# Performance work log

Measured on AMD Instinct MI355X. Metric: run time of the kernel, lower is better.

## Reference

```python
import jax, jax.numpy as jnp
from jax import lax
import numpy as np

MAX_D = 4  # max_displacement


def conv3x3(x, w, b):
    # x: [B,Cin,H,W], w: [Cout,Cin,3,3], SAME padding (pad=1)
    y = lax.conv_general_dilated(
        x, w, window_strides=(1, 1), padding='SAME',
        dimension_numbers=('NCHW', 'OIHW', 'NCHW'))
    return y + b[None, :, None, None]


def compute_cost_volume(f1, f2, d):
    # roll+mask in the torch code == shift with zero padding:
    # cv[idx,h,w] = mean_c f1[c,h,w] * f2[c,h-i,w-j] (zero outside bounds)
    B, C, H, W = f1.shape
    pad = jnp.pad(f2, ((0, 0), (0, 0), (d, d), (d, d)))
    slices = []
    for i in range(-d, d + 1):
        for j in range(-d, d + 1):
            shifted = lax.dynamic_slice(pad, (0, 0, d - i, d - j), (B, C, H, W))
            slices.append((f1 * shifted).sum(axis=1) / C)  # [B,H,W]
    return jnp.stack(slices, axis=1)  # [B,81,H,W]


def setup_inputs() -> dict:
    key = jax.random.key(0)
    ks = jax.random.split(key, 10)
    B, C, H, W = 16, 64, 128, 128
    cv_ch = (2 * MAX_D + 1) ** 2  # 81
    def w_init(k, shape):
        fan_in = shape[1] * shape[2] * shape[3]
        return jax.random.normal(k, shape, dtype=jnp.float32) * np.float32(np.sqrt(2.0 / fan_in))
    return {
        'f1': jax.random.normal(ks[0], (B, C, H, W), dtype=jnp.float32),
        'f2_warped': jax.random.normal(ks[1], (B, C, H, W), dtype=jnp.float32),
        'w1': w_init(ks[2], (128, C + cv_ch, 3, 3)),
        'b1': jnp.zeros((128,), dtype=jnp.float32),
        'w2': w_init(ks[3], (64, 128, 3, 3)),
        'b2': jnp.zeros((64,), dtype=jnp.float32),
        'w3': w_init(ks[4], (32, 64, 3, 3)),
        'b3': jnp.zeros((32,), dtype=jnp.float32),
        'w4': w_init(ks[5], (2, 32, 3, 3)),
        'b4': jnp.zeros((2,), dtype=jnp.float32),
    }


def reference(f1, f2_warped, w1, b1, w2, b2, w3, b3, w4, b4):
    cv = compute_cost_volume(f1, f2_warped, MAX_D)       # [B,81,H,W]
    x = jnp.concatenate([f1, cv], axis=1)                # [B,145,H,W]
    x = jax.nn.relu(conv3x3(x, w1, b1))
    x = jax.nn.relu(conv3x3(x, w2, b2))
    x = jax.nn.relu(conv3x3(x, w3, b3))
    flow = conv3x3(x, w4, b4)                            # [B,2,H,W]
    return flow
```

## Files before the change

kernel.cpp:

```cpp
#include <hip/hip_runtime.h>


typedef __bf16 bf16x8 __attribute__((ext_vector_type(8)));
typedef float f32x4 __attribute__((ext_vector_type(4)));

__device__ __forceinline__ unsigned short f2bf_bits(float f) {
  unsigned int u = __float_as_uint(f);
  unsigned int r = (u + 0x7FFFu + ((u >> 16) & 1u)) >> 16;
  return (unsigned short)r;
}

__device__ __forceinline__ void glds16(const ushort* gp, ushort* lp) {
  __builtin_amdgcn_global_load_lds((const __attribute__((address_space(1))) void*)gp,
                                   (__attribute__((address_space(3))) void*)lp, 16, 0, 0);
}

__global__ void prep_w_kernel(const float* __restrict__ w, uint4* __restrict__ wp,
                              int CIN, int COUT, int CHUNKS, int NFRAG) {
  int idx = blockIdx.x * 256 + threadIdx.x;
  int total = CHUNKS * 9 * NFRAG * 64;
  if (idx >= total) return;
  int lane = idx & 63;
  int fi = idx >> 6;
  int nf = fi % NFRAG;
  int t = fi / NFRAG;
  int rs = t % 9;
  int c = t / 9;
  int co = nf * 16 + (lane & 15);
  int cib = c * 32 + (lane >> 4) * 8;
  union { uint4 q; ushort s[8]; } pk;
#pragma unroll
  for (int e = 0; e < 8; ++e) {
    int ci = cib + e;
    float v = (ci < CIN && co < COUT) ? w[(co * CIN + ci) * 9 + rs] : 0.f;
    pk.s[e] = f2bf_bits(v);
  }
  wp[idx] = pk.q;
}

__global__ __launch_bounds__(256) void pack_f1_kernel(const float* __restrict__ f1,
                                                      ushort* __restrict__ xf1) {
  __shared__ float tile[64][132];
  const int bid = blockIdx.x;
  const int h = bid & 127, b = bid >> 7;
  const int tid = threadIdx.x;
  for (int e = tid; e < 64 * 128; e += 256) {
    int c = e >> 7, w = e & 127;
    tile[c][w] = f1[((b * 64 + c) * 128 + h) * 128 + w];
  }
  __syncthreads();
  const int px = tid >> 1, cgb = (tid & 1) * 4;
  const long base = ((long)(b * 128 + h) * 128 + px) * 64;
#pragma unroll
  for (int e = 0; e < 4; ++e) {
    int c0 = (cgb + e) * 8;
    union { uint4 q; ushort s[8]; } pk;
#pragma unroll
    for (int k = 0; k < 8; ++k) pk.s[k] = f2bf_bits(tile[c0 + k][px]);
    *reinterpret_cast<uint4*>(&xf1[base + c0]) = pk.q;
  }
}

__global__ __launch_bounds__(256)
void cost_volume_mfma_kernel(const ushort* __restrict__ xf1,
                             const ushort* __restrict__ xf2,
                             ushort* __restrict__ xcv) {
  const int bx = blockIdx.x;
  const int idx = bx >> 3;
  const int b = 2 * (bx & 7) + (idx >> 7);
  const int h = idx & 127;
  const int tid = threadIdx.x;
  const int lane = tid & 63;
  const int g = tid >> 6;
  const int l15 = lane & 15;
  const int lg = lane >> 4;

  __shared__ __align__(16) float sC[4][2][16][33];
  __shared__ __align__(16) ushort sO[96][132];

  {
    uint4 z = make_uint4(0u, 0u, 0u, 0u);
    uint4* p = (uint4*)sO;
#pragma unroll
    for (int j = 0; j < 7; ++j) {
      int e = tid + j * 256;
      if (e < 1584) p[e] = z;
    }
  }
  __syncthreads();

  const int w0g = g * 32;
  bf16x8 afr[2][2];
  {
    const ushort* f1p = xf1 + ((long)(b * 128 + h) * 128) * 64;
#pragma unroll
    for (int wt = 0; wt < 2; ++wt)
#pragma unroll
      for (int kc = 0; kc < 2; ++kc) {
        int pix = w0g + wt * 16 + l15;
        afr[wt][kc] = *reinterpret_cast<const bf16x8*>(f1p + pix * 64 + kc * 32 + lg * 8);
      }
  }

  const float inv = 1.0f / 64.0f;
  for (int A = 0; A < 9; ++A) {
    int fr = h - 4 + A;
    if ((unsigned)fr >= 128u) continue;
    const ushort* f2p = xf2 + ((long)(b * 128 + fr) * 128) * 64;
    bf16x8 bfr[3][2];
#pragma unroll
    for (int t = 0; t < 3; ++t)
#pragma unroll
      for (int kc = 0; kc < 2; ++kc) {
        int p = w0g - 4 + t * 16 + l15;
        uint4 v = make_uint4(0u, 0u, 0u, 0u);
        if ((unsigned)p < 128u)
          v = *reinterpret_cast<const uint4*>(f2p + (long)p * 64 + kc * 32 + lg * 8);
        bfr[t][kc] = __builtin_bit_cast(bf16x8, v);
      }
#pragma unroll
    for (int wt = 0; wt < 2; ++wt)
#pragma unroll
      for (int nt = 0; nt < 2; ++nt) {
        f32x4 acc = {0.f, 0.f, 0.f, 0.f};
        acc = __builtin_amdgcn_mfma_f32_16x16x32_bf16(afr[wt][0], bfr[wt + nt][0], acc, 0, 0, 0);
        acc = __builtin_amdgcn_mfma_f32_16x16x32_bf16(afr[wt][1], bfr[wt + nt][1], acc, 0, 0, 0);
#pragma unroll
        for (int j = 0; j < 4; ++j)
          sC[g][wt][lg * 4 + j][nt * 16 + l15] = acc[j];
      }
    const int chb = (8 - A) * 9;
#pragma unroll
    for (int wt = 0; wt < 2; ++wt) {
      int px = w0g + wt * 16 + l15;
#pragma unroll
      for (int u = 0; u < 3; ++u) {
        if (u < ((lg == 3) ? 3 : 2)) {
          int tj = lg * 2 + u;
          float v = sC[g][wt][l15][l15 + 8 - tj];
          sO[chb + tj][px] = f2bf_bits(v * inv);
        }
      }
    }
  }
  __syncthreads();

  uint4* dst = reinterpret_cast<uint4*>(xcv + ((long)(b * 128 + h) * 128) * 96);
#pragma unroll
  for (int j = 0; j < 6; ++j) {
    int t8 = j * 256 + tid;
    int px = t8 / 12;
    int ch0 = (t8 - px * 12) * 8;
    union { uint4 qq; ushort ss[8]; } pk;
#pragma unroll
    for (int k = 0; k < 8; ++k) pk.ss[k] = sO[ch0 + k][px];
    dst[t8] = pk.qq;
  }
}

template <int CA, int CB, int COUT, bool RELU, bool PLANAR>
__global__ __launch_bounds__(512, 2)
void conv_mfma_kernel(const ushort* __restrict__ xa, const ushort* __restrict__ xb,
                      const uint4* __restrict__ wp, const float* __restrict__ bias,
                      void* __restrict__ outv) {
  constexpr int CHUNKS = (CA + CB) / 32;
  constexpr int NFRAG = COUT / 16;
  constexpr int NFW = (NFRAG >= 2) ? NFRAG / 2 : 1;
  constexpr int MFW = (NFRAG >= 2) ? 4 : 2;
  constexpr int SXN = 4 * 130 * 32;
  constexpr int WTQ = 9 * NFRAG * 64;
  constexpr int WTA_Q = 5 * NFRAG * 64;
  constexpr int WTB_Q = 4 * NFRAG * 64;
  constexpr int WIA = (WTA_Q + 511) / 512;
  constexpr int WIB = (WTB_Q + 511) / 512;
  constexpr int SO_STRIDE = COUT + 4;
  constexpr int STAGE_B = PLANAR ? 2048 : 2 * 128 * SO_STRIDE * 2;
  constexpr int SX_B = 2 * SXN * 2;
  constexpr int BASE_B = SX_B + (WTA_Q + WTB_Q) * 16;
  constexpr int ARENA_B = STAGE_B > BASE_B ? STAGE_B : BASE_B;

  __shared__ __align__(16) char arena[ARENA_B];
  ushort* sXa = (ushort*)arena;
  ushort* sWtA = (ushort*)(arena + SX_B);
  ushort* sWtB = (ushort*)(arena + SX_B + WTA_Q * 16);

  const int bx = blockIdx.x;
  const int idx = bx >> 3;
  const int b = 2 * (bx & 7) + (idx >> 6);
  const int h0 = (idx & 63) * 2;
  const int tid = threadIdx.x;
  const int lane = tid & 63;
  const int wid = tid >> 6;
  const int l15 = lane & 15;
  const int lg = lane >> 4;
  const int cg    = (NFRAG >= 2) ? (wid >> 2) : 0;
  const int row   = (NFRAG >= 2) ? ((wid >> 1) & 1) : (wid >> 2);
  const int pbase = (NFRAG >= 2) ? ((wid & 1) * 64) : ((wid & 3) * 32);
  const bool act_wave = ((unsigned)(h0 - 1 + (wid >> 1)) < 128u);

  f32x4 acc[MFW][NFW];
#pragma unroll
  for (int mf = 0; mf < MFW; ++mf)
#pragma unroll
    for (int nf = 0; nf < NFW; ++nf) acc[mf][nf] = {0.f, 0.f, 0.f, 0.f};

  if (tid < 64) {
    int bi = tid >> 5, tr = (tid >> 3) & 3, wz = (tid >> 2) & 1, gq = tid & 3;
    int wl = wz ? 129 : 0;
    *reinterpret_cast<uint4*>(&sXa[bi * SXN + ((tr * 130 + wl) * 4 + gq) * 8]) =
        make_uint4(0u, 0u, 0u, 0u);
  }
  if (h0 == 0 || h0 == 126) {
    const int trz = (h0 == 0) ? 0 : 3;
#pragma unroll
    for (int e = 0; e < 2; ++e) {
      int u = tid + e * 512;
      int bi = u >> 9, k = u & 511;
      *reinterpret_cast<uint4*>(&sXa[bi * SXN + ((trz * 130 + 1) * 4 + k) * 8]) =
          make_uint4(0u, 0u, 0u, 0u);
    }
  }

  auto stage = [&](int c, int bi) {
    const int c0 = c * 32;
    const ushort* src;
    int cst, coff;
    if (CB == 0 || c0 < CA) { src = xa; cst = CA; coff = c0; }
    else                    { src = xb; cst = CB; coff = c0 - CA; }
    const int tr = wid >> 1;
    const int gh = h0 - 1 + tr;
    if ((unsigned)gh < 128u) {
      const ushort* rowp = src + ((long)(b * 128 + gh) * 128) * cst + coff;
#pragma unroll
      for (int t = 0; t < 4; ++t) {
        int s = (wid & 1) * 4 + t;
        int u = s * 64 + lane;
        int wl = 1 + (u >> 2);
        int gq = lane & 3;
        int sw = (wl + (wl >> 2)) & 3;
        const ushort* gp = rowp + (long)(wl - 1) * cst + (gq ^ sw) * 8;
        ushort* lp = &sXa[bi * SXN + ((tr * 130 + 1) * 4 + s * 64) * 8];
        glds16(gp, lp);
      }
    }
  };

  auto stage_wtA = [&](int c) {
    const ushort* src = (const ushort*)(wp + (size_t)c * WTQ);
#pragma unroll
    for (int i = 0; i < WIA; ++i) {
      int e = tid + i * 512;
      if ((WTA_Q % 512) == 0 || e < WTA_Q)
        glds16(src + (size_t)e * 8, sWtA + (size_t)(tid & ~63) * 8 + (size_t)(i * 512) * 8);
    }
  };
  auto stage_wtB = [&](int c) {
    const ushort* src = (const ushort*)(wp + (size_t)c * WTQ + WTA_Q);
#pragma unroll
    for (int i = 0; i < WIB; ++i) {
      int e = tid + i * 512;
      if ((WTB_Q % 512) == 0 || e < WTB_Q)
        glds16(src + (size_t)e * 8, sWtB + (size_t)(tid & ~63) * 8 + (size_t)(i * 512) * 8);
    }
  };

  auto compute = [&](int bi, int rs0, int rs1, const ushort* wbuf) {
#pragma unroll
    for (int rs = rs0; rs < rs1; ++rs) {
      const int r = rs / 3, s = rs % 3;
      const int tr = row + r;
      bf16x8 afr[MFW];
#pragma unroll
      for (int mf = 0; mf < MFW; ++mf) {
        int wl = pbase + mf * 16 + l15 + s;
        int sw = (wl + (wl >> 2)) & 3;
        afr[mf] = *reinterpret_cast<const bf16x8*>(
            &sXa[bi * SXN + ((tr * 130 + wl) * 4 + (lg ^ sw)) * 8]);
      }
      const ushort* wrow = wbuf + (size_t)((rs - rs0) * NFRAG + cg * NFW) * 64 * 8;
#pragma unroll
      for (int nf = 0; nf < NFW; ++nf) {
        bf16x8 bfr = *reinterpret_cast<const bf16x8*>(wrow + (nf * 64 + lane) * 8);
#pragma unroll
        for (int mf = 0; mf < MFW; ++mf)
          acc[mf][nf] = __builtin_amdgcn_mfma_f32_16x16x32_bf16(afr[mf], bfr, acc[mf][nf], 0, 0, 0);
      }
    }
  };

  stage(0, 0);
  stage_wtA(0);
  __syncthreads();

  for (int c = 0; c < CHUNKS; ++c) {
    const int bi = c & 1;
    stage_wtB(c);
    const bool act_issued = (c + 1 < CHUNKS) && act_wave;
    if (c + 1 < CHUNKS) stage(c + 1, bi ^ 1);
    compute(bi, 0, 5, sWtA);
    if (act_issued) asm volatile("s_waitcnt vmcnt(4)" ::: "memory");
    else            asm volatile("s_waitcnt vmcnt(0)" ::: "memory");
    __builtin_amdgcn_s_barrier();
    asm volatile("" ::: "memory");
    if (c + 1 < CHUNKS) stage_wtA(c + 1);
    compute(bi, 5, 9, sWtB);
    asm volatile("s_waitcnt vmcnt(0)" ::: "memory");
    __builtin_amdgcn_s_barrier();
    asm volatile("" ::: "memory");
  }

  if (!PLANAR) {
    ushort* sO = (ushort*)arena;
#pragma unroll
    for (int nf = 0; nf < NFW; ++nf) {
      float bs = bias[cg * NFW * 16 + nf * 16 + l15];
#pragma unroll
      for (int mf = 0; mf < MFW; ++mf) {
        int px2 = row * 128 + pbase + mf * 16 + lg * 4;
#pragma unroll
        for (int j = 0; j < 4; ++j) {
          float v = acc[mf][nf][j] + bs;
          if (RELU) v = fmaxf(v, 0.f);
          sO[(px2 + j) * SO_STRIDE + cg * NFW * 16 + nf * 16 + l15] = f2bf_bits(v);
        }
      }
    }
    __syncthreads();
    constexpr int QPP = COUT / 8;
    uint4* dst = reinterpret_cast<uint4*>((ushort*)outv + ((long)(b * 128 + h0) * 128) * COUT);
#pragma unroll
    for (int t0 = 0; t0 < 2 * 128 * QPP / 512; ++t0) {
      int t = t0 * 512 + tid;
      int px2 = t / QPP;
      int ch0 = (t & (QPP - 1)) * 8;
      union { uint4 qq; ushort ss[8]; } pk;
#pragma unroll
      for (int k = 0; k < 8; ++k) pk.ss[k] = sO[px2 * SO_STRIDE + ch0 + k];
      dst[t] = pk.qq;
    }
  } else {
    float* sF = (float*)arena;
    if (l15 < 2) {
#pragma unroll
      for (int mf = 0; mf < MFW; ++mf) {
        int pxb = pbase + mf * 16 + lg * 4;
#pragma unroll
        for (int j = 0; j < 4; ++j)
          sF[(l15 * 2 + row) * 128 + pxb + j] = acc[mf][0][j] + bias[l15];
      }
    }
    __syncthreads();
    float* out = (float*)outv;
    if (tid < 128) {
      int ch = tid >> 6, r = (tid >> 5) & 1, qx = tid & 31;
      *reinterpret_cast<float4*>(&out[((long)(b * 2 + ch) * 128 + h0 + r) * 128 + qx * 4]) =
          *reinterpret_cast<float4*>(&sF[(ch * 2 + r) * 128 + qx * 4]);
    }
  }
}

extern "C" void kernel_launch(void* const* d_in, const int* in_sizes, int n_in,
                              void* d_out, int out_size, void* d_ws, size_t ws_size,
                              hipStream_t stream) {
  (void)in_sizes; (void)n_in; (void)out_size; (void)ws_size;
  const float* f1 = (const float*)d_in[0];
  const float* f2 = (const float*)d_in[1];
  const float* w1 = (const float*)d_in[2];
  const float* b1 = (const float*)d_in[3];
  const float* w2 = (const float*)d_in[4];
  const float* b2 = (const float*)d_in[5];
  const float* w3 = (const float*)d_in[6];
  const float* b3 = (const float*)d_in[7];
  const float* w4 = (const float*)d_in[8];
  const float* b4 = (const float*)d_in[9];

  char* ws = (char*)d_ws;
  size_t off = 0;
  ushort* xf1 = (ushort*)(ws + off); off += (size_t)262144 * 64 * 2;
  ushort* xcv = (ushort*)(ws + off); off += (size_t)262144 * 96 * 2;
  ushort* x1  = (ushort*)(ws + off); off += (size_t)262144 * 128 * 2;
  ushort* x2  = (ushort*)(ws + off); off += (size_t)262144 * 64 * 2;
  uint4* wp1 = (uint4*)(ws + off); off += (size_t)5 * 9 * 8 * 64 * 16;
  uint4* wp2 = (uint4*)(ws + off); off += (size_t)4 * 9 * 4 * 64 * 16;
  uint4* wp3 = (uint4*)(ws + off); off += (size_t)2 * 9 * 2 * 64 * 16;
  uint4* wp4 = (uint4*)(ws + off); off += (size_t)1 * 9 * 1 * 64 * 16;
  ushort* x3  = xf1;
  ushort* xf2 = x1;

  prep_w_kernel<<<90, 256, 0, stream>>>(w1, wp1, 145, 128, 5, 8);
  prep_w_kernel<<<36, 256, 0, stream>>>(w2, wp2, 128, 64, 4, 4);
  prep_w_kernel<<<9, 256, 0, stream>>>(w3, wp3, 64, 32, 2, 2);
  prep_w_kernel<<<3, 256, 0, stream>>>(w4, wp4, 32, 2, 1, 1);

  pack_f1_kernel<<<2048, 256, 0, stream>>>(f1, xf1);
  pack_f1_kernel<<<2048, 256, 0, stream>>>(f2, xf2);
  cost_volume_mfma_kernel<<<2048, 256, 0, stream>>>(xf1, xf2, xcv);

  conv_mfma_kernel<64, 96, 128, true, false><<<1024, 512, 0, stream>>>(xf1, xcv, wp1, b1, x1);
  conv_mfma_kernel<128, 0, 64, true, false><<<1024, 512, 0, stream>>>(x1, x1, wp2, b2, x2);
  conv_mfma_kernel<64, 0, 32, true, false><<<1024, 512, 0, stream>>>(x2, x2, wp3, b3, x3);
  conv_mfma_kernel<32, 0, 16, false, true><<<1024, 512, 0, stream>>>(x3, x3, wp4, b4, d_out);
}
```

Baseline: 308.0 us.

## Add 4-row conv MFMA kernel with per-tap-row weight double buffering for layers 1-2

Adds a new conv kernel in which each block computes 4 output rows by 64 output channels, staging 6 input rows per 32-channel chunk. Weights are streamed one filter row (3 taps) at a time into double-buffered LDS. Layer 1 is split into two 64-channel halves, and layer 2 runs with half as many blocks. The aim is to reuse each staged activation row across more output rows and to raise MFMA work per weight and activation load, at the cost of extra barriers per chunk. The old kernel's partial vmcnt wait is also replaced with plain __syncthreads, which gives up some load/compute overlap in layers 3-4.

After: 310.6 us. No clear change (+0.8%).

```diff
diff --git a/kernel.cpp b/kernel.cpp
--- a/kernel.cpp
+++ b/kernel.cpp
@@ -155,6 +155,165 @@
 #pragma unroll
     for (int k = 0; k < 8; ++k) pk.ss[k] = sO[ch0 + k][px];
     dst[t8] = pk.qq;
+  }
+}
+
+template <int CA, int CB, int COUT_TOTAL, int HALVES, bool RELU>
+__global__ __launch_bounds__(512, 2)
+void conv_mfma4_kernel(const ushort* __restrict__ xa, const ushort* __restrict__ xb,
+                       const uint4* __restrict__ wp, const float* __restrict__ bias,
+                       ushort* __restrict__ out) {
+  constexpr int CHUNKS = (CA + CB) / 32;
+  constexpr int NFRAGT = COUT_TOTAL / 16;
+
+  __shared__ __align__(16) char arena[74496];
+  uint4* sAct = (uint4*)arena;
+  uint4* sWt = (uint4*)(arena + 49920);
+
+  const int bx = blockIdx.x;
+  const int idx = bx >> 3;
+  int wc, hq, b;
+  if (HALVES == 2) { wc = idx & 1; hq = (idx >> 1) & 31; b = 2 * (bx & 7) + (idx >> 6); }
+  else             { wc = 0;       hq = idx & 31;        b = 2 * (bx & 7) + (idx >> 5); }
+  const int h0 = hq * 4;
+  const int tid = threadIdx.x;
+  const int lane = tid & 63;
+  const int wid = tid >> 6;
+  const int row = wid >> 1;
+  const int ph = wid & 1;
+  const int l15 = lane & 15;
+  const int lg = lane >> 4;
+
+  f32x4 acc[4][4];
+#pragma unroll
+  for (int mf = 0; mf < 4; ++mf)
+#pragma unroll
+    for (int nf = 0; nf < 4; ++nf) acc[mf][nf] = {0.f, 0.f, 0.f, 0.f};
+
+  if (tid < 48) {
+    int tr = tid >> 3, wz = (tid >> 2) & 1, g = tid & 3;
+    sAct[tr * 520 + (wz ? 129 : 0) * 4 + g] = make_uint4(0u, 0u, 0u, 0u);
+  }
+  if (h0 == 0 || h0 == 124) {
+    int trz = (h0 == 0) ? 0 : 5;
+    for (int e = tid; e < 520; e += 512)
+      sAct[trz * 520 + e] = make_uint4(0u, 0u, 0u, 0u);
+  }
+
+  auto stage_act = [&](int c) {
+    const int c0 = c * 32;
+    const ushort* src; int cst, coff;
+    if (CB == 0 || c0 < CA) { src = xa; cst = CA; coff = c0; }
+    else                    { src = xb; cst = CB; coff = c0 - CA; }
+#pragma unroll
+    for (int i = 0; i < 6; ++i) {
+      int sidx = wid + i * 8;
+      int tr = sidx >> 3;
+      int seg = sidx & 7;
+      int gh = h0 - 1 + tr;
+      if ((unsigned)gh < 128u) {
+        int wl = 1 + seg * 16 + (lane >> 2);
+        int g = lane & 3;
+        int sw = (wl + (wl >> 2)) & 3;
+        const ushort* gp = src + ((long)(b * 128 + gh) * 128 + (wl - 1)) * cst + coff + (g ^ sw) * 8;
+        glds16(gp, (ushort*)(sAct + (tr * 520 + 4 + seg * 64)));
+      }
+    }
+  };
+
+  auto stage_wt = [&](int c, int p, int bufsel) {
+    const uint4* srcb = wp + ((size_t)(c * 9 + p * 3) * NFRAGT + wc * 4) * 64;
+#pragma unroll
+    for (int i = 0; i < 2; ++i) {
+      int e = tid + i * 512;
+      if (e < 768) {
+        int rsl = e >> 8;
+        int t = e & 255;
+        glds16((const ushort*)(srcb + (size_t)rsl * (NFRAGT * 64) + t),
+               (ushort*)(sWt + bufsel * 768 + (e & ~63)));
+      }
+    }
+  };
+
+  auto compute = [&](int p, int bufsel) {
+    const int tr = row + p;
+#pragma unroll
+    for (int q = 0; q < 3; ++q) {
+      bf16x8 afr[4];
+#pragma unroll
+      for (int mf = 0; mf < 4; ++mf) {
+        int wl = ph * 64 + mf * 16 + l15 + q;
+        int sw = (wl + (wl >> 2)) & 3;
+        afr[mf] = *reinterpret_cast<const bf16x8*>(
+            (const ushort*)(sAct + ((tr * 130 + wl) * 4 + (lg ^ sw))));
+      }
+      const uint4* wpiece = sWt + bufsel * 768 + q * 256;
+#pragma unroll
+      for (int nf = 0; nf < 4; ++nf) {
+        bf16x8 bfr = __builtin_bit_cast(bf16x8, wpiece[nf * 64 + lane]);
+#pragma unroll
+        for (int mf = 0; mf < 4; ++mf)
+          acc[mf][nf] = __builtin_amdgcn_mfma_f32_16x16x32_bf16(afr[mf], bfr, acc[mf][nf], 0, 0, 0);
+      }
+    }
+  };
+
+  stage_act(0);
+  stage_wt(0, 0, 0);
+  asm volatile("s_waitcnt vmcnt(0)" ::: "memory");
+  __builtin_amdgcn_s_barrier();
+  asm volatile("" ::: "memory");
+
+  for (int c = 0; c < CHUNKS; ++c) {
+    const int P0 = (3 * c) & 1, P1 = (3 * c + 1) & 1;
+    stage_wt(c, 1, P1);
+    compute(0, P0);
+    asm volatile("s_waitcnt vmcnt(0)" ::: "memory");
+    __builtin_amdgcn_s_barrier();
+    asm volatile("" ::: "memory");
+    stage_wt(c, 2, P0);
+    compute(1, P1);
+    asm volatile("s_waitcnt vmcnt(0)" ::: "memory");
+    __builtin_amdgcn_s_barrier();
+    asm volatile("" ::: "memory");
+    if (c + 1 < CHUNKS) stage_wt(c + 1, 0, P1);
+    compute(2, P0);
+    asm volatile("s_waitcnt lgkmcnt(0)" ::: "memory");
+    __builtin_amdgcn_s_barrier();
+    asm volatile("" ::: "memory");
+    if (c + 1 < CHUNKS) stage_act(c + 1);
+    asm volatile("s_waitcnt vmcnt(0)" ::: "memory");
+    __builtin_amdgcn_s_barrier();
+    asm volatile("" ::: "memory");
+  }
+
+  ushort* sO = (ushort*)arena;
+#pragma unroll
+  for (int nf = 0; nf < 4; ++nf) {
+    float bs = bias[wc * 64 + nf * 16 + l15];
+#pragma unroll
+    for (int mf = 0; mf < 4; ++mf) {
+      int px2 = row * 128 + ph * 64 + mf * 16 + lg * 4;
+#pragma unroll
+      for (int j = 0; j < 4; ++j) {
+        float v = acc[mf][nf][j] + bs;
+        if (RELU) v = fmaxf(v, 0.f);
+        sO[(px2 + j) * 68 + nf * 16 + l15] = f2bf_bits(v);
+      }
+    }
+  }
+  __syncthreads();
+#pragma unroll
+  for (int t0 = 0; t0 < 8; ++t0) {
+    int t = t0 * 512 + tid;
+    int px2 = t >> 3;
+    int ch0 = (t & 7) * 8;
+    union { uint4 qq; ushort ss[8]; } pk;
+#pragma unroll
+    for (int k = 0; k < 8; ++k) pk.ss[k] = sO[px2 * 68 + ch0 + k];
+    int rowg = px2 >> 7, px = px2 & 127;
+    long oidx = ((long)(b * 128 + h0 + rowg) * 128 + px) * COUT_TOTAL + wc * 64 + ch0;
+    *reinterpret_cast<uint4*>(out + oidx) = pk.qq;
   }
 }
 
@@ -196,7 +355,6 @@
   const int cg    = (NFRAG >= 2) ? (wid >> 2) : 0;
   const int row   = (NFRAG >= 2) ? ((wid >> 1) & 1) : (wid >> 2);
   const int pbase = (NFRAG >= 2) ? ((wid & 1) * 64) : ((wid & 3) * 32);
-  const bool act_wave = ((unsigned)(h0 - 1 + (wid >> 1)) < 128u);
 
   f32x4 acc[MFW][NFW];
 #pragma unroll
@@ -295,18 +453,12 @@
   for (int c = 0; c < CHUNKS; ++c) {
     const int bi = c & 1;
     stage_wtB(c);
-    const bool act_issued = (c + 1 < CHUNKS) && act_wave;
     if (c + 1 < CHUNKS) stage(c + 1, bi ^ 1);
     compute(bi, 0, 5, sWtA);
-    if (act_issued) asm volatile("s_waitcnt vmcnt(4)" ::: "memory");
-    else            asm volatile("s_waitcnt vmcnt(0)" ::: "memory");
-    __builtin_amdgcn_s_barrier();
-    asm volatile("" ::: "memory");
+    __syncthreads();
     if (c + 1 < CHUNKS) stage_wtA(c + 1);
     compute(bi, 5, 9, sWtB);
-    asm volatile("s_waitcnt vmcnt(0)" ::: "memory");
-    __builtin_amdgcn_s_barrier();
-    asm volatile("" ::: "memory");
+    __syncthreads();
   }
 
   if (!PLANAR) {
@@ -396,8 +548,8 @@
   pack_f1_kernel<<<2048, 256, 0, stream>>>(f2, xf2);
   cost_volume_mfma_kernel<<<2048, 256, 0, stream>>>(xf1, xf2, xcv);
 
-  conv_mfma_kernel<64, 96, 128, true, false><<<1024, 512, 0, stream>>>(xf1, xcv, wp1, b1, x1);
-  conv_mfma_kernel<128, 0, 64, true, false><<<1024, 512, 0, stream>>>(x1, x1, wp2, b2, x2);
+  conv_mfma4_kernel<64, 96, 128, 2, true><<<1024, 512, 0, stream>>>(xf1, xcv, wp1, b1, x1);
+  conv_mfma4_kernel<128, 0, 64, 1, true><<<512, 512, 0, stream>>>(x1, x1, wp2, b2, x2);
   conv_mfma_kernel<64, 0, 32, true, false><<<1024, 512, 0, stream>>>(x2, x2, wp3, b3, x3);
   conv_mfma_kernel<32, 0, 16, false, true><<<1024, 512, 0, stream>>>(x3, x3, wp4, b4, d_out);
 }
```
